# Performance work log

Hardware: AMD Instinct MI355X
Metric: run time of the kernel (lower is better)

## Reference

```python
import jax, jax.numpy as jnp
import numpy as np

DIM = 1024
DEPTH = 6
HEADS = 16
DH = 64
INNER = HEADS * DH  # 1024
MLP = 4096
B, N = 2, 2048
SCALE = DH ** (-0.5)  # 0.125; module divides softmax output by this (x8)
EPS = 1e-5


def setup_inputs() -> dict:
    key = jax.random.key(0)
    ks = jax.random.split(key, 5)
    s = jnp.float32(0.02)
    return {
        "x": jax.random.normal(ks[0], (B, N, DIM), dtype=jnp.float32),
        "ln1_g": jnp.ones((DEPTH, DIM), jnp.float32),
        "ln1_b": jnp.zeros((DEPTH, DIM), jnp.float32),
        "w_qkv": jax.random.normal(ks[1], (DEPTH, DIM, 3 * INNER), jnp.float32) * s,
        "w_out": jax.random.normal(ks[2], (DEPTH, INNER, DIM), jnp.float32) * s,
        "b_out": jnp.zeros((DEPTH, DIM), jnp.float32),
        "ln2_g": jnp.ones((DEPTH, DIM), jnp.float32),
        "ln2_b": jnp.zeros((DEPTH, DIM), jnp.float32),
        "w1": jax.random.normal(ks[3], (DEPTH, DIM, MLP), jnp.float32) * s,
        "b1": jnp.zeros((DEPTH, MLP), jnp.float32),
        "w2": jax.random.normal(ks[4], (DEPTH, MLP, DIM), jnp.float32) * s,
        "b2": jnp.zeros((DEPTH, DIM), jnp.float32),
    }


def _layernorm(x, g, b):
    m = x.mean(-1, keepdims=True)
    v = ((x - m) ** 2).mean(-1, keepdims=True)
    return (x - m) * jax.lax.rsqrt(v + EPS) * g + b


def _attention(x, w_qkv, w_out, b_out):
    b, n, _ = x.shape
    qkv = x @ w_qkv  # [b, n, 3*inner]
    q, k, v = jnp.split(qkv, 3, axis=-1)

    def heads(t):
        return t.reshape(b, n, HEADS, DH).transpose(0, 2, 1, 3)  # [b,h,n,d]

    q, k, v = heads(q), heads(k), heads(v)
    # Faithful to source: softmax of UNSCALED logits, then divide by scale.
    score = jax.nn.softmax(jnp.einsum("bhqd,bhkd->bhqk", q, k), axis=-1) / SCALE
    o = jnp.einsum("bhqk,bhkd->bhqd", score, v)
    o = o.transpose(0, 2, 1, 3).reshape(b, n, INNER)
    return o @ w_out + b_out


def reference(x, ln1_g, ln1_b, w_qkv, w_out, b_out, ln2_g, ln2_b, w1, b1, w2, b2):
    def layer(h, p):
        g1, bb1, wq, wo, bo, g2, bb2, ww1, bw1, ww2, bw2 = p
        h = h + _attention(_layernorm(h, g1, bb1), wq, wo, bo)
        f = _layernorm(h, g2, bb2) @ ww1 + bw1
        f = jax.nn.gelu(f, approximate=False)  # nn.GELU default = exact erf
        h = h + f @ ww2 + bw2
        return h, None

    out, _ = jax.lax.scan(
        layer, x, (ln1_g, ln1_b, w_qkv, w_out, b_out, ln2_g, ln2_b, w1, b1, w2, b2)
    )
    return out
```

## Files before the change

### kernel.cpp

```cpp
#include <hip/hip_runtime.h>
#include <cstdint>

typedef __attribute__((ext_vector_type(4))) float f32x4;
typedef __attribute__((ext_vector_type(8))) short short8;
typedef __attribute__((ext_vector_type(4))) short short4v;
typedef _Float16 half8v __attribute__((ext_vector_type(8)));

__device__ __forceinline__ unsigned short f2h(float x) {
  _Float16 h = (_Float16)x;
  return __builtin_bit_cast(unsigned short, h);
}
__device__ __forceinline__ unsigned int pk2(float a, float b) {
  auto h = __builtin_amdgcn_cvt_pkrtz(a, b);
  return __builtin_bit_cast(unsigned int, h);
}

template <typename V>
__device__ __forceinline__ auto mfma_impl(V a, V b, f32x4 c, int)
    -> decltype(__builtin_amdgcn_mfma_f32_16x16x32_f16(a, b, c, 0, 0, 0)) {
  return __builtin_amdgcn_mfma_f32_16x16x32_f16(a, b, c, 0, 0, 0);
}
template <typename V>
__device__ __forceinline__ f32x4 mfma_impl(V a, V b, f32x4 c, long) {
  return __builtin_amdgcn_mfma_f32_16x16x32_f16(
      __builtin_bit_cast(half8v, a), __builtin_bit_cast(half8v, b), c, 0, 0, 0);
}
__device__ __forceinline__ f32x4 MFMA(short8 a, short8 b, f32x4 c) {
  return mfma_impl(a, b, c, 0);
}

__device__ __forceinline__ void load_lds16(const void* g, void* l) {
  __builtin_amdgcn_global_load_lds(
      (__attribute__((address_space(1))) void*)(uintptr_t)g,
      (__attribute__((address_space(3))) void*)l, 16, 0, 0);
}

__global__ __launch_bounds__(256) void ln_f16_kernel(
    const float* __restrict__ X, const float* __restrict__ gam,
    const float* __restrict__ bet, unsigned short* __restrict__ Y) {
  __shared__ float red[8];
  const int row = blockIdx.x, t = threadIdx.x;
  const float4 v = ((const float4*)(X + (size_t)row * 1024))[t];
  float s = v.x + v.y + v.z + v.w;
#pragma unroll
  for (int o = 32; o >= 1; o >>= 1) s += __shfl_xor(s, o, 64);
  if ((t & 63) == 0) red[t >> 6] = s;
  __syncthreads();
  const float mean = (red[0] + red[1] + red[2] + red[3]) * (1.0f / 1024.0f);
  const float dx = v.x - mean, dy = v.y - mean, dz = v.z - mean, dw = v.w - mean;
  float ss = dx * dx + dy * dy + dz * dz + dw * dw;
#pragma unroll
  for (int o = 32; o >= 1; o >>= 1) ss += __shfl_xor(ss, o, 64);
  if ((t & 63) == 0) red[4 + (t >> 6)] = ss;
  __syncthreads();
  const float var = (red[4] + red[5] + red[6] + red[7]) * (1.0f / 1024.0f);
  const float rstd = rsqrtf(var + 1e-5f);
  const float4 gg = ((const float4*)gam)[t];
  const float4 bb = ((const float4*)bet)[t];
  ushort4 o4;
  o4.x = f2h(dx * rstd * gg.x + bb.x);
  o4.y = f2h(dy * rstd * gg.y + bb.y);
  o4.z = f2h(dz * rstd * gg.z + bb.z);
  o4.w = f2h(dw * rstd * gg.w + bb.w);
  ((ushort4*)(Y + (size_t)row * 1024))[t] = o4;
}

__global__ __launch_bounds__(256) void transpose_all_kernel(
    const float* __restrict__ wq, const float* __restrict__ wo,
    const float* __restrict__ w1, const float* __restrict__ w2,
    unsigned short* __restrict__ wtq, unsigned short* __restrict__ wto,
    unsigned short* __restrict__ wt1, unsigned short* __restrict__ wt2) {
  __shared__ float t[32][33];
  int i = blockIdx.x;
  const float* W; unsigned short* WT; int K, N;
  if (i < 3072)      { W = wq; WT = wtq; K = 1024; N = 3072; }
  else if (i < 4096) { i -= 3072; W = wo; WT = wto; K = 1024; N = 1024; }
  else if (i < 8192) { i -= 4096; W = w1; WT = wt1; K = 1024; N = 4096; }
  else               { i -= 8192; W = w2; WT = wt2; K = 4096; N = 1024; }
  const int nt = N >> 5;
  const int n0 = (i % nt) * 32, k0 = (i / nt) * 32;
  const int tx = threadIdx.x, ty = threadIdx.y;
#pragma unroll
  for (int j = 0; j < 4; ++j)
    t[ty + 8 * j][tx] = W[(size_t)(k0 + ty + 8 * j) * N + n0 + tx];
  __syncthreads();
#pragma unroll
  for (int j = 0; j < 4; ++j)
    WT[(size_t)(n0 + ty + 8 * j) * K + k0 + tx] = f2h(t[tx][ty + 8 * j]);
}

template <int BM, int EPI>
__global__ __launch_bounds__(256, BM == 64 ? 3 : 2) void gemm_f16_kernel(
    const unsigned short* __restrict__ A, const unsigned short* __restrict__ BT,
    void* Cout, const float* __restrict__ bias, const float* __restrict__ res,
    unsigned short* __restrict__ vtout, int gx, int M, int N, int K) {
  constexpr int BN = 128, BK = 64;
  constexpr int MR = BM / 32;
  constexpr int ACH = BM * BK / 8;
  constexpr int BCH = BN * BK / 8;
  __shared__ alignas(16) unsigned short a_sh[2][BM * BK];
  __shared__ alignas(16) unsigned short b_sh[2][BN * BK];
  const int tid = threadIdx.x;
  const int w = tid >> 6, lane = tid & 63, g = lane >> 4, lm = lane & 15;
  int bid = blockIdx.x;
  const int cpx = gridDim.x >> 3;
  bid = (bid & 7) * cpx + (bid >> 3);
  const int m0 = (bid / gx) * BM, n0 = (bid % gx) * BN;
  const int wm = (w >> 1) * (BM / 2), wn = (w & 1) * 64;
  f32x4 acc[MR][4] = {};
  const int nsteps = K >> 6;

  auto stage = [&](int buf, int kk) {
#pragma unroll
    for (int c0 = 0; c0 < ACH; c0 += 256) {
      const int c = c0 + tid, row = c >> 3;
      const int sc = (c & 7) ^ (row & 7);
      const int cb = c0 + (tid & 192);
      load_lds16(A + (size_t)(m0 + row) * K + kk + sc * 8, &a_sh[buf][cb * 8]);
    }
#pragma unroll
    for (int c0 = 0; c0 < BCH; c0 += 256) {
      const int c = c0 + tid, row = c >> 3;
      const int sc = (c & 7) ^ (row & 7);
      const int cb = c0 + (tid & 192);
      load_lds16(BT + (size_t)(n0 + row) * K + kk + sc * 8, &b_sh[buf][cb * 8]);
    }
  };

  stage(0, 0);
  __syncthreads();
  int cur = 0;
  for (int step = 0; step < nsteps; ++step) {
    if (step + 1 < nsteps) stage(cur ^ 1, (step + 1) * BK);
#pragma unroll
    for (int kc = 0; kc < 2; ++kc) {
      short8 af[MR], bfr[4];
#pragma unroll
      for (int i = 0; i < MR; ++i) {
        const int r = wm + i * 16 + lm;
        af[i] = *(const short8*)&a_sh[cur][r * 64 + (((kc << 2) | g) ^ (r & 7)) * 8];
      }
#pragma unroll
      for (int j = 0; j < 4; ++j) {
        const int r = wn + j * 16 + lm;
        bfr[j] = *(const short8*)&b_sh[cur][r * 64 + (((kc << 2) | g) ^ (r & 7)) * 8];
      }
#pragma unroll
      for (int i = 0; i < MR; ++i)
#pragma unroll
        for (int j = 0; j < 4; ++j)
          acc[i][j] = MFMA(af[i], bfr[j], acc[i][j]);
    }
    if (step + 1 < nsteps) {
      __syncthreads();
      cur ^= 1;
    }
  }

  if (EPI == 3 && n0 >= 2048) {
#pragma unroll
    for (int i = 0; i < MR; ++i) {
      const int row = m0 + wm + i * 16 + g * 4;
      const int bb = row >> 11, rin = row & 2047;
#pragma unroll
      for (int j = 0; j < 4; ++j) {
        const int vcol = n0 + wn + j * 16 + lm - 2048;
        ushort4 o4;
        o4.x = f2h(acc[i][j][0]);
        o4.y = f2h(acc[i][j][1]);
        o4.z = f2h(acc[i][j][2]);
        o4.w = f2h(acc[i][j][3]);
        *(ushort4*)&vtout[((size_t)bb * 1024 + vcol) * 2048 + rin] = o4;
      }
    }
    return;
  }

#pragma unroll
  for (int i = 0; i < MR; ++i) {
    const int row = m0 + wm + i * 16 + g * 4;
#pragma unroll
    for (int j = 0; j < 4; ++j) {
      const int col = n0 + wn + j * 16 + lm;
#pragma unroll
      for (int r = 0; r < 4; ++r) {
        const float v = acc[i][j][r];
        const size_t idx = (size_t)(row + r) * N + col;
        if (EPI == 0 || EPI == 3) {
          ((unsigned short*)Cout)[idx] = f2h(v);
        } else if (EPI == 1) {
          const float xx = v + bias[col];
          ((unsigned short*)Cout)[idx] =
              f2h(0.5f * xx * (1.0f + erff(xx * 0.70710678118654752f)));
        } else {
          ((float*)Cout)[idx] = res[idx] + v + bias[col];
        }
      }
    }
  }
}

__global__ __launch_bounds__(1024) void attn_kernel(
    const unsigned short* __restrict__ qkv, const unsigned short* __restrict__ vt,
    unsigned short* __restrict__ obuf) {
  constexpr int PK = 72;
  constexpr int PV = 68;
  __shared__ alignas(16) unsigned short Ks[64 * PK];
  __shared__ alignas(16) unsigned short VsT[64 * PV];
  const int tid = threadIdx.x;
  const int w = tid >> 6, lane = tid & 63, g = lane >> 4, lm = lane & 15;
  const int qbase = blockIdx.x * 256, h = blockIdx.y, b = blockIdx.z;
  const size_t rowbase = (size_t)b * 2048;
  const int sr = (tid & 511) >> 3, sc = tid & 7;
  const bool doK = tid < 512;

  const unsigned short* qp =
      qkv + (rowbase + qbase + w * 16 + lm) * 3072 + h * 64 + g * 8;
  short8 qf[2];
  qf[0] = *(const short8*)qp;
  qf[1] = *(const short8*)(qp + 32);

  const unsigned short* sptr = doK
      ? qkv + (rowbase + sr) * 3072 + 1024 + h * 64 + sc * 8
      : vt + ((size_t)b * 1024 + h * 64 + sr) * 2048 + sc * 8;
  const int sdst = doK ? sr * PK + sc * 8 : sr * PV + sc * 8;
  unsigned short* sbase = doK ? Ks : VsT;
  uint4 sreg;
  auto load_tile = [&](int n) {
    sreg = doK ? *(const uint4*)(sptr + (size_t)n * 64 * 3072)
               : *(const uint4*)(sptr + n * 64);
  };
  auto write_tile = [&]() { *(uint4*)&sbase[sdst] = sreg; };

  load_tile(0);
  float mrun = -1e30f, lrun = 0.0f;
  f32x4 accO[4] = {};

  for (int n = 0; n < 32; ++n) {
    __syncthreads();
    write_tile();
    __syncthreads();
    if (n + 1 < 32) load_tile(n + 1);

    f32x4 sf[4] = {};
    __builtin_amdgcn_s_setprio(1);
#pragma unroll
    for (int s2 = 0; s2 < 2; ++s2)
#pragma unroll
      for (int i = 0; i < 4; ++i) {
        const short8 kf = *(const short8*)&Ks[(i * 16 + lm) * PK + s2 * 32 + g * 8];
        sf[i] = MFMA(kf, qf[s2], sf[i]);
      }
    __builtin_amdgcn_s_setprio(0);

    float tmax = -1e30f;
#pragma unroll
    for (int i = 0; i < 4; ++i)
#pragma unroll
      for (int r = 0; r < 4; ++r) tmax = fmaxf(tmax, sf[i][r]);
    tmax = fmaxf(tmax, __shfl_xor(tmax, 16, 64));
    tmax = fmaxf(tmax, __shfl_xor(tmax, 32, 64));
    const float mnew = fmaxf(mrun, tmax);
    const float scale = __expf(mrun - mnew);
    float p[4][4];
    float psum = 0.0f;
#pragma unroll
    for (int i = 0; i < 4; ++i)
#pragma unroll
      for (int r = 0; r < 4; ++r) {
        p[i][r] = __expf(sf[i][r] - mnew);
        psum += p[i][r];
      }
    psum += __shfl_xor(psum, 16, 64);
    psum += __shfl_xor(psum, 32, 64);
    lrun = lrun * scale + psum;
    mrun = mnew;
#pragma unroll
    for (int t = 0; t < 4; ++t) accO[t] = accO[t] * scale;

    uint4 pbu[2];
#pragma unroll
    for (int blk = 0; blk < 2; ++blk) {
      pbu[blk].x = pk2(p[2 * blk][0], p[2 * blk][1]);
      pbu[blk].y = pk2(p[2 * blk][2], p[2 * blk][3]);
      pbu[blk].z = pk2(p[2 * blk + 1][0], p[2 * blk + 1][1]);
      pbu[blk].w = pk2(p[2 * blk + 1][2], p[2 * blk + 1][3]);
    }

    __builtin_amdgcn_s_setprio(1);
#pragma unroll
    for (int blk = 0; blk < 2; ++blk) {
      const short8 pbv = __builtin_bit_cast(short8, pbu[blk]);
#pragma unroll
      for (int t = 0; t < 4; ++t) {
        const int base = (16 * t + lm) * PV + 32 * blk + 4 * g;
        const short4v vlo = *(const short4v*)&VsT[base];
        const short4v vhi = *(const short4v*)&VsT[base + 16];
        const short8 vf = {vlo[0], vlo[1], vlo[2], vlo[3],
                           vhi[0], vhi[1], vhi[2], vhi[3]};
        accO[t] = MFMA(vf, pbv, accO[t]);
      }
    }
    __builtin_amdgcn_s_setprio(0);
  }

  const float inv = 8.0f / lrun;
  const size_t orow = rowbase + qbase + w * 16 + lm;
#pragma unroll
  for (int t = 0; t < 4; ++t) {
    ushort4 o4;
    o4.x = f2h(accO[t][0] * inv);
    o4.y = f2h(accO[t][1] * inv);
    o4.z = f2h(accO[t][2] * inv);
    o4.w = f2h(accO[t][3] * inv);
    *(ushort4*)&obuf[orow * 1024 + h * 64 + t * 16 + g * 4] = o4;
  }
}

extern "C" void kernel_launch(void* const* d_in, const int* in_sizes, int n_in,
                              void* d_out, int out_size, void* d_ws, size_t ws_size,
                              hipStream_t stream) {
  const float* x     = (const float*)d_in[0];
  const float* ln1_g = (const float*)d_in[1];
  const float* ln1_b = (const float*)d_in[2];
  const float* w_qkv = (const float*)d_in[3];
  const float* w_out = (const float*)d_in[4];
  const float* b_out = (const float*)d_in[5];
  const float* ln2_g = (const float*)d_in[6];
  const float* ln2_b = (const float*)d_in[7];
  const float* w1    = (const float*)d_in[8];
  const float* b1    = (const float*)d_in[9];
  const float* w2    = (const float*)d_in[10];
  const float* b2    = (const float*)d_in[11];
  float* h = (float*)d_out;

  char* ws = (char*)d_ws;
  const size_t MB = 1u << 20;
  unsigned short* xn   = (unsigned short*)(ws);
  unsigned short* ob   = (unsigned short*)(ws + 8 * MB);
  unsigned short* qkvb = (unsigned short*)(ws + 16 * MB);
  unsigned short* mid  = (unsigned short*)(ws + 40 * MB);
  unsigned short* wt   = (unsigned short*)(ws + 72 * MB);
  unsigned short* wtq = wt;
  unsigned short* wto = wt + 3145728;
  unsigned short* wt1 = wt + 4194304;
  unsigned short* wt2 = wt + 8388608;

  hipError_t e0 = hipMemcpyAsync(h, x, (size_t)4096 * 1024 * sizeof(float),
                                 hipMemcpyDeviceToDevice, stream);
  (void)e0;

  const dim3 tb(32, 8);
  for (int L = 0; L < 6; ++L) {
    const float* Lg1 = ln1_g + L * 1024;
    const float* Lb1 = ln1_b + L * 1024;
    const float* Lwq = w_qkv + (size_t)L * 1024 * 3072;
    const float* Lwo = w_out + (size_t)L * 1024 * 1024;
    const float* Lbo = b_out + L * 1024;
    const float* Lg2 = ln2_g + L * 1024;
    const float* Lb2 = ln2_b + L * 1024;
    const float* Lw1 = w1 + (size_t)L * 1024 * 4096;
    const float* Lb1m = b1 + L * 4096;
    const float* Lw2 = w2 + (size_t)L * 4096 * 1024;
    const float* Lb2m = b2 + L * 1024;

    transpose_all_kernel<<<12288, tb, 0, stream>>>(
        Lwq, Lwo, Lw1, Lw2, wtq, wto, wt1, wt2);

    ln_f16_kernel<<<4096, 256, 0, stream>>>(h, Lg1, Lb1, xn);
    gemm_f16_kernel<128, 3><<<768, 256, 0, stream>>>(
        xn, wtq, qkvb, nullptr, nullptr, mid, 24, 4096, 3072, 1024);
    attn_kernel<<<dim3(8, 16, 2), 1024, 0, stream>>>(qkvb, mid, ob);
    gemm_f16_kernel<64, 2><<<512, 256, 0, stream>>>(
        ob, wto, h, Lbo, h, nullptr, 8, 4096, 1024, 1024);

    ln_f16_kernel<<<4096, 256, 0, stream>>>(h, Lg2, Lb2, xn);
    gemm_f16_kernel<128, 1><<<1024, 256, 0, stream>>>(
        xn, wt1, mid, Lb1m, nullptr, nullptr, 32, 4096, 4096, 1024);
    gemm_f16_kernel<64, 2><<<512, 256, 0, stream>>>(
        mid, wt2, h, Lb2m, h, nullptr, 8, 4096, 1024, 4096);
  }
  (void)in_sizes; (void)n_in; (void)out_size; (void)ws_size;
}
```

Before: 1.614 ms.

## Double-buffer attention K/V tiles, halve block size, use exp2 with prescaled Q

The attention kernel now uses 512-thread blocks over 128 queries, which doubles the grid to 512 blocks. Each thread loads both a K and a V chunk into double-buffered LDS, so there is one barrier per tile instead of two, and the next tile's global load is prefetched two iterations ahead. Q is prescaled by log2(e) so the softmax can use exp2f instead of __expf. This should reduce barrier stalls and improve occupancy and load latency hiding, at the cost of doubled LDS, more registers per thread, and an extra fp16 rounding of the scaled Q.

```diff
diff --git a/kernel.cpp b/kernel.cpp
--- a/kernel.cpp
+++ b/kernel.cpp
@@ -9,6 +9,9 @@
 __device__ __forceinline__ unsigned short f2h(float x) {
   _Float16 h = (_Float16)x;
   return __builtin_bit_cast(unsigned short, h);
+}
+__device__ __forceinline__ float h2f(unsigned short u) {
+  return (float)__builtin_bit_cast(_Float16, u);
 }
 __device__ __forceinline__ unsigned int pk2(float a, float b) {
   auto h = __builtin_amdgcn_cvt_pkrtz(a, b);
@@ -200,47 +203,60 @@
   }
 }
 
-__global__ __launch_bounds__(1024) void attn_kernel(
+__global__ __launch_bounds__(512) void attn_kernel(
     const unsigned short* __restrict__ qkv, const unsigned short* __restrict__ vt,
     unsigned short* __restrict__ obuf) {
   constexpr int PK = 72;
   constexpr int PV = 68;
-  __shared__ alignas(16) unsigned short Ks[64 * PK];
-  __shared__ alignas(16) unsigned short VsT[64 * PV];
+  __shared__ alignas(16) unsigned short Ks[2][64 * PK];
+  __shared__ alignas(16) unsigned short VsT[2][64 * PV];
   const int tid = threadIdx.x;
   const int w = tid >> 6, lane = tid & 63, g = lane >> 4, lm = lane & 15;
-  const int qbase = blockIdx.x * 256, h = blockIdx.y, b = blockIdx.z;
+  const int qbase = blockIdx.x * 128, h = blockIdx.y, b = blockIdx.z;
   const size_t rowbase = (size_t)b * 2048;
-  const int sr = (tid & 511) >> 3, sc = tid & 7;
-  const bool doK = tid < 512;
+  const int r0 = tid >> 3, cc = tid & 7;
+  const float LOG2E = 1.44269504088896f;
 
   const unsigned short* qp =
       qkv + (rowbase + qbase + w * 16 + lm) * 3072 + h * 64 + g * 8;
+  const short8 q0 = *(const short8*)qp;
+  const short8 q1 = *(const short8*)(qp + 32);
   short8 qf[2];
-  qf[0] = *(const short8*)qp;
-  qf[1] = *(const short8*)(qp + 32);
-
-  const unsigned short* sptr = doK
-      ? qkv + (rowbase + sr) * 3072 + 1024 + h * 64 + sc * 8
-      : vt + ((size_t)b * 1024 + h * 64 + sr) * 2048 + sc * 8;
-  const int sdst = doK ? sr * PK + sc * 8 : sr * PV + sc * 8;
-  unsigned short* sbase = doK ? Ks : VsT;
-  uint4 sreg;
+#pragma unroll
+  for (int j = 0; j < 4; ++j) {
+    ((unsigned*)&qf[0])[j] = pk2(h2f((unsigned short)q0[2 * j]) * LOG2E,
+                                 h2f((unsigned short)q0[2 * j + 1]) * LOG2E);
+    ((unsigned*)&qf[1])[j] = pk2(h2f((unsigned short)q1[2 * j]) * LOG2E,
+                                 h2f((unsigned short)q1[2 * j + 1]) * LOG2E);
+  }
+
+  const unsigned short* kptr = qkv + (rowbase + r0) * 3072 + 1024 + h * 64 + cc * 8;
+  const unsigned short* vtp = vt + ((size_t)b * 1024 + h * 64 + r0) * 2048 + cc * 8;
+  uint4 kreg, vreg;
   auto load_tile = [&](int n) {
-    sreg = doK ? *(const uint4*)(sptr + (size_t)n * 64 * 3072)
-               : *(const uint4*)(sptr + n * 64);
+    kreg = *(const uint4*)(kptr + (size_t)n * 64 * 3072);
+    vreg = *(const uint4*)(vtp + n * 64);
   };
-  auto write_tile = [&]() { *(uint4*)&sbase[sdst] = sreg; };
+  auto write_tile = [&](int buf) {
+    *(uint4*)&Ks[buf][r0 * PK + cc * 8] = kreg;
+    *(uint4*)&VsT[buf][r0 * PV + cc * 8] = vreg;
+  };
 
   load_tile(0);
+  write_tile(0);
+  load_tile(1);
+  __syncthreads();
+
   float mrun = -1e30f, lrun = 0.0f;
   f32x4 accO[4] = {};
 
   for (int n = 0; n < 32; ++n) {
-    __syncthreads();
-    write_tile();
-    __syncthreads();
-    if (n + 1 < 32) load_tile(n + 1);
+    const int cur = n & 1;
+    if (n) __syncthreads();
+    if (n + 1 < 32) {
+      write_tile(cur ^ 1);
+      if (n + 2 < 32) load_tile(n + 2);
+    }
 
     f32x4 sf[4] = {};
     __builtin_amdgcn_s_setprio(1);
@@ -248,7 +264,7 @@
     for (int s2 = 0; s2 < 2; ++s2)
 #pragma unroll
       for (int i = 0; i < 4; ++i) {
-        const short8 kf = *(const short8*)&Ks[(i * 16 + lm) * PK + s2 * 32 + g * 8];
+        const short8 kf = *(const short8*)&Ks[cur][(i * 16 + lm) * PK + s2 * 32 + g * 8];
         sf[i] = MFMA(kf, qf[s2], sf[i]);
       }
     __builtin_amdgcn_s_setprio(0);
@@ -261,14 +277,14 @@
     tmax = fmaxf(tmax, __shfl_xor(tmax, 16, 64));
     tmax = fmaxf(tmax, __shfl_xor(tmax, 32, 64));
     const float mnew = fmaxf(mrun, tmax);
-    const float scale = __expf(mrun - mnew);
+    const float scale = exp2f(mrun - mnew);
     float p[4][4];
     float psum = 0.0f;
 #pragma unroll
     for (int i = 0; i < 4; ++i)
 #pragma unroll
       for (int r = 0; r < 4; ++r) {
-        p[i][r] = __expf(sf[i][r] - mnew);
+        p[i][r] = exp2f(sf[i][r] - mnew);
         psum += p[i][r];
       }
     psum += __shfl_xor(psum, 16, 64);
@@ -294,8 +310,8 @@
 #pragma unroll
       for (int t = 0; t < 4; ++t) {
         const int base = (16 * t + lm) * PV + 32 * blk + 4 * g;
-        const short4v vlo = *(const short4v*)&VsT[base];
-        const short4v vhi = *(const short4v*)&VsT[base + 16];
+        const short4v vlo = *(const short4v*)&VsT[cur][base];
+        const short4v vhi = *(const short4v*)&VsT[cur][base + 16];
         const short8 vf = {vlo[0], vlo[1], vlo[2], vlo[3],
                            vhi[0], vhi[1], vhi[2], vhi[3]};
         accO[t] = MFMA(vf, pbv, accO[t]);
@@ -370,7 +386,7 @@
     ln_f16_kernel<<<4096, 256, 0, stream>>>(h, Lg1, Lb1, xn);
     gemm_f16_kernel<128, 3><<<768, 256, 0, stream>>>(
         xn, wtq, qkvb, nullptr, nullptr, mid, 24, 4096, 3072, 1024);
-    attn_kernel<<<dim3(8, 16, 2), 1024, 0, stream>>>(qkvb, mid, ob);
+    attn_kernel<<<dim3(16, 16, 2), 512, 0, stream>>>(qkvb, mid, ob);
     gemm_f16_kernel<64, 2><<<512, 256, 0, stream>>>(
         ob, wto, h, Lbo, h, nullptr, 8, 4096, 1024, 1024);
 
```

New measurement: 1.671 ms. 3.5% more time.
